# Performance work log

Hardware: AMD Instinct MI355X
Metric: run time of the kernel (lower is better)

Reference implementation:

```python
import jax, jax.numpy as jnp
import numpy as np

VOCAB = 50257
D_MODEL = 1024
BATCH = 4
SEQ = 4096


def setup_inputs() -> dict:
    key = jax.random.key(0)
    k_ids, k_w = jax.random.split(key)
    input = jax.random.randint(k_ids, (BATCH, SEQ), 0, VOCAB, dtype=jnp.int32)
    # Linear(vocab, d_model, bias=False) weight: [d_model, vocab]
    W = jax.random.normal(k_w, (D_MODEL, VOCAB), dtype=jnp.float32) * (1.0 / np.sqrt(VOCAB))
    return {"input": input, "W": W}


def reference(input, W):
    # one_hot(input, vocab) @ W.T  ==  gather columns of W
    # out[b, s, :] = W[:, input[b, s]]  -> shape [B, S, d_model]
    return jnp.take(W.T, input, axis=0)
```

## Files before the change

kernel.cpp:

```cpp
#include <hip/hip_runtime.h>
#include <stdint.h>

#define VOCAB   50257
#define DMODEL  1024
#define VWIN    256
#define NB      ((VOCAB + VWIN - 1) / VWIN)
#define DCH     16
#define CAP     1024

#define WS_CNT   0
#define WS_LIST  256

typedef __attribute__((address_space(1))) const void* gas_ptr;
typedef __attribute__((address_space(3))) void*       las_ptr;

__global__ __launch_bounds__(256) void partition_kernel(
    const int* __restrict__ ids, int* __restrict__ ws, int n_tokens)
{
    __shared__ int cnt;
    const int vwin = blockIdx.x;
    const int tid  = threadIdx.x;
    if (tid == 0) cnt = 0;
    __syncthreads();
    for (int t = tid; t < n_tokens; t += 256) {
        int id = ids[t];
        if ((id >> 8) == vwin) {
            int pos = atomicAdd(&cnt, 1);
            if (pos < CAP)
                ws[WS_LIST + vwin * CAP + pos] =
                    (int)(((uint32_t)(id & 255) << 16) | (uint32_t)t);
        }
    }
    __syncthreads();
    if (tid == 0) ws[WS_CNT + vwin] = min(cnt, CAP);
}

__global__ __launch_bounds__(256) void emit_kernel(
    const float* __restrict__ W, const int* __restrict__ ws,
    float* __restrict__ out)
{
    __shared__ float tile[DCH][VWIN + 1];

    const int vwin = blockIdx.x;
    const int dk   = blockIdx.y * DCH;
    const int v0   = vwin << 8;
    const int tid  = threadIdx.x;
    const int lane = tid & 63;
    const int w    = tid >> 6;

    if (vwin != NB - 1) {
#pragma unroll
        for (int r2 = 0; r2 < 4; ++r2) {
            const int row = w * 4 + r2;
            const float* gsrc = W + (size_t)(dk + row) * VOCAB + v0 + lane;
            float* ldst = &tile[row][0];
#pragma unroll
            for (int q = 0; q < 4; ++q) {
                __builtin_amdgcn_global_load_lds(
                    (gas_ptr)(gsrc + q * 64), (las_ptr)(ldst + q * 64),
                    4, 0, 0);
            }
        }
    } else {
        const int limit = VOCAB - v0;
        for (int e = tid; e < DCH * VWIN; e += 256) {
            int r = e >> 8, c = e & 255;
            if (c < limit)
                tile[r][c] = W[(size_t)(dk + r) * VOCAB + v0 + c];
        }
    }

    const int total = ws[WS_CNT + vwin];
    const int* __restrict__ list = ws + WS_LIST + vwin * CAP;

    asm volatile("s_waitcnt vmcnt(0)" ::: "memory");
    __syncthreads();

    const int g = lane >> 2;
    const int j = lane & 3;

    for (int i = w * 16; i < total; i += 64) {
        int idx = i + g;
        if (idx < total) {
            uint32_t packed = (uint32_t)list[idx];
            int t   = (int)(packed & 0xFFFFu);
            int col = (int)(packed >> 16);
            float4 v;
            v.x = tile[j * 4 + 0][col];
            v.y = tile[j * 4 + 1][col];
            v.z = tile[j * 4 + 2][col];
            v.w = tile[j * 4 + 3][col];
            *(float4*)(out + (size_t)t * DMODEL + dk + j * 4) = v;
        }
    }
}

extern "C" void kernel_launch(void* const* d_in, const int* in_sizes, int n_in,
                              void* d_out, int out_size, void* d_ws, size_t ws_size,
                              hipStream_t stream) {
    const int*   ids = (const int*)d_in[0];
    const float* W   = (const float*)d_in[1];
    float*       out = (float*)d_out;
    int*         ws  = (int*)d_ws;

    const int n_tokens = in_sizes[0];

    partition_kernel<<<NB, 256, 0, stream>>>(ids, ws, n_tokens);

    dim3 grid(NB, DMODEL / DCH);
    emit_kernel<<<grid, 256, 0, stream>>>(W, ws, out);
}
```

Before: 344.5 us.

## Use 16-byte direct-to-LDS loads with skewed layout and 32-row tiles

Each emit block now stages 32 rows of W per vocab window with 512 threads instead of 16 rows with 256. Most of the staging uses 16-byte global_load_lds instructions rather than 4-byte ones. Rows of W are not 16-byte aligned because VOCAB is odd, so each row is loaded from an aligned address just before its start, stored into a skewed LDS layout, and the tail is filled by a second 4-byte load. The goal is fewer load instructions and better use of the memory pipe, at the cost of more complex indexing, redundant tail loads, and doubled LDS per block, which may lower occupancy.

New measurement: 333.7 us. -3.1%, faster.

```diff
diff --git a/kernel.cpp b/kernel.cpp
--- a/kernel.cpp
+++ b/kernel.cpp
@@ -5,11 +5,17 @@
 #define DMODEL  1024
 #define VWIN    256
 #define NB      ((VOCAB + VWIN - 1) / VWIN)
-#define DCH     16
+#define DCH     32
 #define CAP     1024
 
 #define WS_CNT   0
 #define WS_LIST  256
+
+#define LSTRIDE 272
+__device__ __forceinline__ int lidx(int r, int k) {
+    return r * LSTRIDE + ((r >> 2) << 2) + k;
+}
+#define LDS_FLOATS (31 * LSTRIDE + 7 * 4 + 259 + 1)
 
 typedef __attribute__((address_space(1))) const void* gas_ptr;
 typedef __attribute__((address_space(3))) void*       las_ptr;
@@ -35,11 +41,11 @@
     if (tid == 0) ws[WS_CNT + vwin] = min(cnt, CAP);
 }
 
-__global__ __launch_bounds__(256) void emit_kernel(
+__global__ __launch_bounds__(512) void emit_kernel(
     const float* __restrict__ W, const int* __restrict__ ws,
     float* __restrict__ out)
 {
-    __shared__ float tile[DCH][VWIN + 1];
+    __shared__ float tile[LDS_FLOATS];
 
     const int vwin = blockIdx.x;
     const int dk   = blockIdx.y * DCH;
@@ -50,23 +56,25 @@
 
     if (vwin != NB - 1) {
 #pragma unroll
-        for (int r2 = 0; r2 < 4; ++r2) {
-            const int row = w * 4 + r2;
-            const float* gsrc = W + (size_t)(dk + row) * VOCAB + v0 + lane;
-            float* ldst = &tile[row][0];
-#pragma unroll
-            for (int q = 0; q < 4; ++q) {
-                __builtin_amdgcn_global_load_lds(
-                    (gas_ptr)(gsrc + q * 64), (las_ptr)(ldst + q * 64),
-                    4, 0, 0);
-            }
+        for (int rr = 0; rr < 4; ++rr) {
+            const int row  = w * 4 + rr;
+            const int grow = dk + row;
+            const int mis  = grow & 3;
+            const size_t gbase = (size_t)grow * VOCAB + v0;
+            __builtin_amdgcn_global_load_lds(
+                (gas_ptr)(W + gbase - mis + (size_t)lane * 4),
+                (las_ptr)(tile + lidx(row, 0)), 16, 0, 0);
+            __builtin_amdgcn_global_load_lds(
+                (gas_ptr)(W + gbase + 192 + lane),
+                (las_ptr)(tile + lidx(row, 192 + mis)), 4, 0, 0);
         }
     } else {
         const int limit = VOCAB - v0;
-        for (int e = tid; e < DCH * VWIN; e += 256) {
+        for (int e = tid; e < DCH * VWIN; e += 512) {
             int r = e >> 8, c = e & 255;
             if (c < limit)
-                tile[r][c] = W[(size_t)(dk + r) * VOCAB + v0 + c];
+                tile[lidx(r, c + (r & 3))] =
+                    W[(size_t)(dk + r) * VOCAB + v0 + c];
         }
     }
 
@@ -76,22 +84,19 @@
     asm volatile("s_waitcnt vmcnt(0)" ::: "memory");
     __syncthreads();
 
-    const int g = lane >> 2;
-    const int j = lane & 3;
+    const int g = lane >> 3;
+    const int j = lane & 7;
 
-    for (int i = w * 16; i < total; i += 64) {
-        int idx = i + g;
-        if (idx < total) {
-            uint32_t packed = (uint32_t)list[idx];
-            int t   = (int)(packed & 0xFFFFu);
-            int col = (int)(packed >> 16);
-            float4 v;
-            v.x = tile[j * 4 + 0][col];
-            v.y = tile[j * 4 + 1][col];
-            v.z = tile[j * 4 + 2][col];
-            v.w = tile[j * 4 + 3][col];
-            *(float4*)(out + (size_t)t * DMODEL + dk + j * 4) = v;
-        }
+    for (int i = w * 8 + g; i < total; i += 64) {
+        uint32_t packed = (uint32_t)list[i];
+        int t   = (int)(packed & 0xFFFFu);
+        int col = (int)(packed >> 16);
+        float4 v;
+        v.x = tile[lidx(4 * j + 0, col + 0)];
+        v.y = tile[lidx(4 * j + 1, col + 1)];
+        v.z = tile[lidx(4 * j + 2, col + 2)];
+        v.w = tile[lidx(4 * j + 3, col + 3)];
+        *(float4*)(out + (size_t)t * DMODEL + dk + j * 4) = v;
     }
 }
 
@@ -108,5 +113,5 @@
     partition_kernel<<<NB, 256, 0, stream>>>(ids, ws, n_tokens);
 
     dim3 grid(NB, DMODEL / DCH);
-    emit_kernel<<<grid, 256, 0, stream>>>(W, ws, out);
+    emit_kernel<<<grid, 512, 0, stream>>>(W, ws, out);
 }
```
